# Kernel tuning notes

Hardware: AMD Instinct MI355X
Metric: run time of the kernel (lower is better)

## Reference

```python
import jax, jax.numpy as jnp
import numpy as np

N, F, LATENT = 4096, 64, 32
ENC = [128, 64]
DEC = [64, 96, 128]
B = 8


def _glorot(key, shape):
    s = jnp.sqrt(2.0 / (shape[0] + shape[-1]))
    return jax.random.normal(key, shape, jnp.float32) * s


def setup_inputs() -> dict:
    key = jax.random.key(0)
    ks = jax.random.split(key, 12)
    # Random symmetric graph (avg degree ~16), then spektral-style preprocessing:
    # normalized_laplacian: L = I - D^-1/2 A D^-1/2 ; rescale_laplacian(lmax=2): 2/lmax*L - I = L - I
    rng = np.random.default_rng(0)
    A = (rng.random((N, N)) < (16.0 / N)).astype(np.float32)
    A = np.maximum(A, A.T)
    np.fill_diagonal(A, 0.0)
    d = A.sum(1)
    dis = 1.0 / np.sqrt(np.maximum(d, 1.0))
    L = np.eye(N, dtype=np.float32) - dis[:, None] * A * dis[None, :]
    A0 = (L - np.eye(N, dtype=np.float32)).astype(np.float32)
    return dict(
        x=jax.random.normal(ks[0], (B, N, F), jnp.float32),
        eps=jax.random.normal(ks[1], (B, N // 4, LATENT), jnp.float32),
        A0=jnp.asarray(A0),
        W1=_glorot(ks[2], (F, ENC[0])), b1=jnp.zeros((ENC[0],), jnp.float32),
        p1=jax.random.normal(ks[3], (ENC[0],), jnp.float32),
        W2=_glorot(ks[4], (ENC[0], ENC[1])), b2=jnp.zeros((ENC[1],), jnp.float32),
        p2=jax.random.normal(ks[5], (ENC[1],), jnp.float32),
        Wlat=_glorot(ks[6], (ENC[1], 2 * LATENT)), blat=jnp.zeros((2 * LATENT,), jnp.float32),
        Wd0=_glorot(ks[7], (LATENT, DEC[0])), bd0=jnp.zeros((DEC[0],), jnp.float32),
        Wd1=_glorot(ks[8], (DEC[0], DEC[1])), bd1=jnp.zeros((DEC[1],), jnp.float32),
        Wd2=_glorot(ks[9], (DEC[1], DEC[2])), bd2=jnp.zeros((DEC[2],), jnp.float32),
        Wout=_glorot(ks[10], (DEC[2], F)), bout=jnp.zeros((F,), jnp.float32),
    )


def _gcn(x, A, W, b):
    # spektral GCNConv with pre-normalized adjacency: A @ x @ W + b
    return A @ (x @ W) + b


def _topk_pool(x, A, p):
    # spektral TopKPool (Graph U-Net): y = x.p/||p||, keep top ratio=0.5 nodes,
    # gate kept features with tanh(y), pool adjacency A' = A[idx][:, idx].
    y = x @ (p / jnp.linalg.norm(p))                 # [n]
    k = x.shape[0] // 2
    idx = jnp.sort(jax.lax.top_k(y, k)[1])           # node-order preserving
    xp = x[idx] * jnp.tanh(y[idx])[:, None]          # [k, c]
    Ap = A[idx][:, idx]                              # [k, k]
    return xp, Ap, idx


def _unpool(x, idx, n_old):
    # TopKUnpool: scatter pooled features back to their original node slots, zeros elsewhere.
    return jnp.zeros((n_old, x.shape[1]), x.dtype).at[idx].set(x)


def reference(x, eps, A0, W1, b1, p1, W2, b2, p2, Wlat, blat,
              Wd0, bd0, Wd1, bd1, Wd2, bd2, Wout, bout):
    def single(x1, eps1):
        # ---- encoder ----
        h = jax.nn.relu(_gcn(x1, A0, W1, b1))        # [N, 128]
        h, A1, idx1 = _topk_pool(h, A0, p1)          # [N/2, 128]
        h = jax.nn.relu(_gcn(h, A1, W2, b2))         # [N/2, 64]
        h, A2, idx2 = _topk_pool(h, A1, p2)          # [N/4, 64]
        hl = _gcn(h, A2, Wlat, blat)                 # [N/4, 2*LATENT]
        mean, logvar = jnp.split(hl, 2, axis=-1)
        # ---- reparameterize ----
        z = mean + jnp.exp(0.5 * logvar) * eps1
        # ---- decoder ----
        d = jax.nn.relu(_gcn(z, A2, Wd0, bd0))       # [N/4, 64]
        d = _unpool(d, idx2, N // 2)
        d = jax.nn.relu(_gcn(d, A1, Wd1, bd1))       # [N/2, 96]
        d = _unpool(d, idx1, N)
        d = jax.nn.relu(_gcn(d, A0, Wd2, bd2))       # [N, 128]
        out = jax.nn.softplus(_gcn(d, A0, Wout, bout))  # [N, F]
        return out, mean, logvar

    return jax.vmap(single)(x, eps)
```

## Files before the change

### kernel.cpp

```cpp
#include <hip/hip_runtime.h>
#include <hip/hip_bf16.h>

#define NN 4096
#define BB 8
#define LAT 32
#define ELLCAP 128

__global__ __launch_bounds__(256) void ell_build(const float* __restrict__ A,
                                                 int* __restrict__ col,
                                                 float* __restrict__ val,
                                                 int* __restrict__ nnz) {
  int w = threadIdx.x >> 6;
  int lane = threadIdx.x & 63;
  int row = blockIdx.x * 4 + w;
  const float* ar = A + (size_t)row * NN;
  int base = 0;
  for (int i = 0; i < NN; i += 256) {
    float4 a = *(const float4*)&ar[i + lane * 4];
    int cnt = (a.x != 0.f) + (a.y != 0.f) + (a.z != 0.f) + (a.w != 0.f);
    int x = cnt;
#pragma unroll
    for (int off = 1; off < 64; off <<= 1) {
      int y = __shfl_up(x, off, 64);
      if (lane >= off) x += y;
    }
    int total = __shfl(x, 63, 64);
    int p = base + x - cnt;
    float av[4] = {a.x, a.y, a.z, a.w};
#pragma unroll
    for (int u = 0; u < 4; u++) {
      if (av[u] != 0.f) {
        if (p < ELLCAP) {
          col[(size_t)row * ELLCAP + p] = i + lane * 4 + u;
          val[(size_t)row * ELLCAP + p] = av[u];
        }
        p++;
      }
    }
    base += total;
  }
  if (lane == 0) nnz[row] = base < ELLCAP ? base : ELLCAP;
}

__global__ void pnorm_kernel(const float* __restrict__ p1, const float* __restrict__ p2,
                             float* __restrict__ invn) {
  int lane = threadIdx.x;
  float s1 = 0.f, s2 = 0.f;
  for (int i = lane; i < 128; i += 64) s1 += p1[i] * p1[i];
  { float v = p2[lane]; s2 = v * v; }
  for (int off = 32; off; off >>= 1) { s1 += __shfl_down(s1, off); s2 += __shfl_down(s2, off); }
  if (lane == 0) { invn[0] = rsqrtf(s1); invn[1] = rsqrtf(s2); }
}

template <int CT>
__global__ __launch_bounds__(256) void gemm_kernel(
    const float* __restrict__ in, const float* __restrict__ W, float* __restrict__ out,
    int M, int K, long inB, long outB, const int* __restrict__ map, int mapB,
    const float* __restrict__ gateY, long gyB, const float* __restrict__ invn, int which) {
  const int C = CT * 32;
  const int KT = 32, LDI = KT + 4;
  extern __shared__ float lds[];
  float* Wl = lds;
  float* inT = lds + KT * C;
  int b = blockIdx.y;
  const float* inb = in + (size_t)b * inB;
  float* outb = out + (size_t)b * outB;
  const int* mapb = map ? map + (size_t)b * mapB : nullptr;
  int tx = threadIdx.x, ty = threadIdx.y;
  int row0 = blockIdx.x * 32;
  float acc[4][CT];
#pragma unroll
  for (int i = 0; i < 4; i++)
#pragma unroll
    for (int j = 0; j < CT; j++) acc[i][j] = 0.f;
  for (int kt = 0; kt < K; kt += KT) {
    int kc = (K - kt < KT) ? (K - kt) : KT;
    for (int r = ty; r < kc; r += 8)
      for (int c = tx; c < C; c += 32) Wl[r * C + c] = W[(size_t)(kt + r) * C + c];
    for (int r = ty; r < 32; r += 8) {
      int grow = row0 + r;
      int src = grow;
      if (mapb) src = mapb[grow];
      if (src >= 0) {
        float gate = 1.f;
        if (gateY) gate = tanhf(gateY[(size_t)b * gyB + src] * invn[which]);
        const float* ib = inb + (size_t)src * K + kt;
        for (int k = tx; k < kc; k += 32) inT[r * LDI + k] = ib[k] * gate;
      } else {
        for (int k = tx; k < kc; k += 32) inT[r * LDI + k] = 0.f;
      }
    }
    __syncthreads();
    for (int k = 0; k < kc; k += 4) {
      float4 a[4];
#pragma unroll
      for (int i = 0; i < 4; i++) a[i] = *(const float4*)&inT[(ty + i * 8) * LDI + k];
#pragma unroll
      for (int kk = 0; kk < 4; kk++) {
#pragma unroll
        for (int j = 0; j < CT; j++) {
          float w = Wl[(k + kk) * C + tx + j * 32];
#pragma unroll
          for (int i = 0; i < 4; i++) {
            float av = ((const float*)&a[i])[kk];
            acc[i][j] = fmaf(av, w, acc[i][j]);
          }
        }
      }
    }
    __syncthreads();
  }
#pragma unroll
  for (int i = 0; i < 4; i++) {
    int grow = row0 + ty + i * 8;
#pragma unroll
    for (int j = 0; j < CT; j++) outb[(size_t)grow * C + tx + j * 32] = acc[i][j];
  }
}

template <int C>
__global__ __launch_bounds__(128) void spmm_vec_kernel(
    const int* __restrict__ ecol, const float* __restrict__ evals, const int* __restrict__ ennz,
    const int* __restrict__ rowmap, int rowmapB,
    const int* __restrict__ colinv, int colinvB,
    const float* __restrict__ Y, long yB, const float* __restrict__ bias,
    float* __restrict__ out, long outB, int act,
    const float* __restrict__ eps, float* __restrict__ meanOut,
    float* __restrict__ logvarOut, float* __restrict__ zOut,
    const float* __restrict__ pvec, float* __restrict__ yOut, long yOutB) {
  constexpr int L = C / 4;
  constexpr int R = 128 / L;
  __shared__ int scol[R][ELLCAP];
  __shared__ float sval[R][ELLCAP];
  int bid = blockIdx.x;
  int rb = bid >> 3, b = bid & 7;
  int t = threadIdx.x;
  int rloc = t / L, lane = t % L;
  int row = rb * R + rloc;
  int grow = rowmap ? rowmap[(size_t)b * rowmapB + row] : row;
  int n = ennz[grow];
  const int* cp = ecol + (size_t)grow * ELLCAP;
  const float* vp = evals + (size_t)grow * ELLCAP;
  const int* ci = colinv ? colinv + (size_t)b * colinvB : nullptr;
  for (int e = lane; e < n; e += L) {
    int c = cp[e];
    int li = ci ? ci[c] : c;
    float w = vp[e];
    if (li < 0) { li = 0; w = 0.f; }
    scol[rloc][e] = li;
    sval[rloc][e] = w;
  }
  __syncthreads();
  const float* Yb = Y + (size_t)b * yB;
  float4 acc = {0.f, 0.f, 0.f, 0.f};
  int e = 0;
  for (; e + 8 <= n; e += 8) {
    float4 v[8];
    float w[8];
#pragma unroll
    for (int u = 0; u < 8; u++) {
      w[u] = sval[rloc][e + u];
      v[u] = *(const float4*)&Yb[(size_t)scol[rloc][e + u] * C + lane * 4];
    }
#pragma unroll
    for (int u = 0; u < 8; u++) {
      acc.x = fmaf(w[u], v[u].x, acc.x);
      acc.y = fmaf(w[u], v[u].y, acc.y);
      acc.z = fmaf(w[u], v[u].z, acc.z);
      acc.w = fmaf(w[u], v[u].w, acc.w);
    }
  }
  for (; e < n; e++) {
    float w = sval[rloc][e];
    float4 v = *(const float4*)&Yb[(size_t)scol[rloc][e] * C + lane * 4];
    acc.x = fmaf(w, v.x, acc.x);
    acc.y = fmaf(w, v.y, acc.y);
    acc.z = fmaf(w, v.z, acc.z);
    acc.w = fmaf(w, v.w, acc.w);
  }
  float4 bi = *(const float4*)&bias[lane * 4];
  acc.x += bi.x; acc.y += bi.y; acc.z += bi.z; acc.w += bi.w;
  if (act == 1) {
    acc.x = fmaxf(acc.x, 0.f); acc.y = fmaxf(acc.y, 0.f);
    acc.z = fmaxf(acc.z, 0.f); acc.w = fmaxf(acc.w, 0.f);
  } else if (act == 2) {
    acc.x = fmaxf(acc.x, 0.f) + log1pf(expf(-fabsf(acc.x)));
    acc.y = fmaxf(acc.y, 0.f) + log1pf(expf(-fabsf(acc.y)));
    acc.z = fmaxf(acc.z, 0.f) + log1pf(expf(-fabsf(acc.z)));
    acc.w = fmaxf(acc.w, 0.f) + log1pf(expf(-fabsf(acc.w)));
  } else if (act == 3) {
    int wl = t & 63;
    float4 lv;
    lv.x = __shfl(acc.x, wl + 8, 64);
    lv.y = __shfl(acc.y, wl + 8, 64);
    lv.z = __shfl(acc.z, wl + 8, 64);
    lv.w = __shfl(acc.w, wl + 8, 64);
    size_t o = ((size_t)b * 1024 + row) * LAT;
    if (lane < 8) {
      *(float4*)&meanOut[o + lane * 4] = acc;
      float4 ep = *(const float4*)&eps[o + lane * 4];
      float4 z;
      z.x = fmaf(expf(0.5f * lv.x), ep.x, acc.x);
      z.y = fmaf(expf(0.5f * lv.y), ep.y, acc.y);
      z.z = fmaf(expf(0.5f * lv.z), ep.z, acc.z);
      z.w = fmaf(expf(0.5f * lv.w), ep.w, acc.w);
      *(float4*)&zOut[o + lane * 4] = z;
    } else {
      *(float4*)&logvarOut[o + (lane - 8) * 4] = acc;
    }
    return;
  }
  *(float4*)&out[(size_t)b * outB + (size_t)row * C + lane * 4] = acc;
  if (yOut) {
    float4 pv = *(const float4*)&pvec[lane * 4];
    float part = acc.x * pv.x + acc.y * pv.y + acc.z * pv.z + acc.w * pv.w;
#pragma unroll
    for (int off = L / 2; off > 0; off >>= 1) part += __shfl_down(part, off, 64);
    if (lane == 0) yOut[(size_t)b * yOutB + row] = part;
  }
}

__global__ void spmm_kernel(
    const int* __restrict__ ecol, const float* __restrict__ evals, const int* __restrict__ ennz,
    const int* __restrict__ rowmap, int rowmapB,
    const int* __restrict__ colinv, int colinvB,
    const float* __restrict__ Y, long yB, const float* __restrict__ bias,
    float* __restrict__ out, long outB, int C, int act) {
  __shared__ int scol[ELLCAP];
  __shared__ float sval[ELLCAP];
  int bid = blockIdx.x;
  int row = bid >> 3, b = bid & 7;
  int t = threadIdx.x;
  int grow = rowmap ? rowmap[(size_t)b * rowmapB + row] : row;
  int n = ennz[grow];
  const int* cp = ecol + (size_t)grow * ELLCAP;
  const float* vp = evals + (size_t)grow * ELLCAP;
  const int* ci = colinv ? colinv + (size_t)b * colinvB : nullptr;
  for (int e = t; e < n; e += C) {
    int c = cp[e];
    int li = ci ? ci[c] : c;
    float w = vp[e];
    if (li < 0) { li = 0; w = 0.f; }
    scol[e] = li;
    sval[e] = w;
  }
  __syncthreads();
  const float* Yb = Y + (size_t)b * yB;
  float acc = 0.f;
  int e = 0;
  for (; e + 8 <= n; e += 8) {
    const float* ap[8];
    float w[8], pv[8];
#pragma unroll
    for (int u = 0; u < 8; u++) {
      ap[u] = Yb + (size_t)scol[e + u] * C + t;
      w[u] = sval[e + u];
    }
#pragma unroll
    for (int u = 0; u < 8; u++) pv[u] = *ap[u];
#pragma unroll
    for (int u = 0; u < 8; u++) acc = fmaf(w[u], pv[u], acc);
  }
  for (; e < n; e++) acc = fmaf(sval[e], Yb[(size_t)scol[e] * C + t], acc);
  acc += bias[t];
  if (act == 1) acc = fmaxf(acc, 0.f);
  out[(size_t)b * outB + (size_t)row * C + t] = acc;
}

__global__ __launch_bounds__(1024) void topk_kernel(
    const float* __restrict__ yIn, int yB, int n, int k,
    const int* __restrict__ prevIdx, int prevB,
    int* __restrict__ idxLoc, int idxB,
    int* __restrict__ invLoc, int invB,
    int* __restrict__ gIdx, int gIdxB,
    int* __restrict__ gInv, int gInvB) {
  __shared__ unsigned int sk[4096];
  __shared__ unsigned int hist[256];
  __shared__ int si[1024];
  __shared__ int s_bin, s_cum;
  int b = blockIdx.x, tid = threadIdx.x;
  const float* y = yIn + (size_t)b * yB;
  for (int i = tid; i < n; i += 1024) {
    unsigned u = __float_as_uint(y[i]);
    sk[i] = (u & 0x80000000u) ? ~u : (u | 0x80000000u);
  }
  int* invb = invLoc + (size_t)b * invB;
  for (int i = tid; i < n; i += 1024) invb[i] = -1;
  int* ginvb = gInv ? gInv + (size_t)b * gInvB : nullptr;
  if (ginvb)
    for (int i = tid; i < NN; i += 1024) ginvb[i] = -1;
  __syncthreads();
  unsigned prefix = 0;
  int kneed = k, countGt = 0;
  for (int shift = 24; shift >= 0; shift -= 8) {
    if (tid < 256) hist[tid] = 0;
    __syncthreads();
    unsigned pmask = (shift == 24) ? 0u : (0xFFFFFFFFu << (shift + 8));
    for (int i = tid; i < n; i += 1024) {
      unsigned key = sk[i];
      if ((key & pmask) == prefix) atomicAdd(&hist[(key >> shift) & 255], 1u);
    }
    __syncthreads();
    if (tid < 256) si[tid] = (int)hist[tid];
    __syncthreads();
    for (int off = 1; off < 256; off <<= 1) {
      int v = 0;
      if (tid < 256) { v = si[tid]; if (tid + off < 256) v += si[tid + off]; }
      __syncthreads();
      if (tid < 256) si[tid] = v;
      __syncthreads();
    }
    if (tid < 256) {
      int cumAbove = (tid < 255) ? si[tid + 1] : 0;
      if (cumAbove < kneed && kneed <= cumAbove + (int)hist[tid]) {
        s_bin = tid;
        s_cum = cumAbove;
      }
    }
    __syncthreads();
    int bin = s_bin, cumAbove = s_cum;
    countGt += cumAbove;
    kneed -= cumAbove;
    prefix |= ((unsigned)bin << shift);
    __syncthreads();
  }
  unsigned tkey = prefix;
  int needEq = k - countGt;
  int ipt = n >> 10;
  int i0 = tid * ipt;
  int locGt = 0, locEq = 0;
  for (int u = 0; u < ipt; u++) {
    unsigned key = sk[i0 + u];
    locGt += (key > tkey) ? 1 : 0;
    locEq += (key == tkey) ? 1 : 0;
  }
  int comb = (locGt << 13) | locEq;
  si[tid] = comb;
  __syncthreads();
  for (int off = 1; off < 1024; off <<= 1) {
    int vv = si[tid];
    int add = (tid >= off) ? si[tid - off] : 0;
    __syncthreads();
    si[tid] = vv + add;
    __syncthreads();
  }
  int excl = si[tid] - comb;
  int gtB = excl >> 13;
  int eqB = excl & 0x1FFF;
  int* idxb = idxLoc + (size_t)b * idxB;
  int* gidxb = gIdx ? gIdx + (size_t)b * gIdxB : nullptr;
  const int* prevb = prevIdx ? prevIdx + (size_t)b * prevB : nullptr;
  for (int u = 0; u < ipt; u++) {
    int i = i0 + u;
    unsigned key = sk[i];
    bool g = key > tkey;
    bool e = (key == tkey);
    bool sel = g || (e && eqB < needEq);
    if (sel) {
      int pos = gtB + (eqB < needEq ? eqB : needEq);
      idxb[pos] = i;
      invb[i] = pos;
      int gi = prevb ? prevb[i] : i;
      if (gidxb) gidxb[pos] = gi;
      if (ginvb) ginvb[gi] = pos;
    }
    gtB += g ? 1 : 0;
    eqB += e ? 1 : 0;
  }
}

static inline void launch_gemm(const float* in, const float* W, float* out, int M, int K, int C,
                               long inB, long outB, const int* map, int mapB, hipStream_t s,
                               const float* gateY = nullptr, long gyB = 0,
                               const float* invn = nullptr, int which = 0) {
  dim3 g(M / 32, BB), bl(32, 8);
  size_t lds = (size_t)(32 * C + 32 * 36) * 4;
  if (C == 64)
    gemm_kernel<2><<<g, bl, lds, s>>>(in, W, out, M, K, inB, outB, map, mapB, gateY, gyB, invn, which);
  else if (C == 96)
    gemm_kernel<3><<<g, bl, lds, s>>>(in, W, out, M, K, inB, outB, map, mapB, gateY, gyB, invn, which);
  else
    gemm_kernel<4><<<g, bl, lds, s>>>(in, W, out, M, K, inB, outB, map, mapB, gateY, gyB, invn, which);
}

static inline void launch_spmm(const int* ecol, const float* evals, const int* ennz,
                               const int* rowmap, int rowmapB, const int* colinv, int colinvB,
                               const float* Y, long yB, const float* bias, float* out, long outB,
                               int M, int C, int act, hipStream_t s,
                               const float* eps = nullptr, float* meanOut = nullptr,
                               float* lvOut = nullptr, float* zOut = nullptr,
                               const float* pvec = nullptr, float* yOut = nullptr, long yOutB = 0) {
  if (C == 128) {
    spmm_vec_kernel<128><<<dim3((M / 4) * BB), dim3(128), 0, s>>>(
        ecol, evals, ennz, rowmap, rowmapB, colinv, colinvB, Y, yB, bias, out, outB, act,
        eps, meanOut, lvOut, zOut, pvec, yOut, yOutB);
  } else if (C == 64) {
    spmm_vec_kernel<64><<<dim3((M / 8) * BB), dim3(128), 0, s>>>(
        ecol, evals, ennz, rowmap, rowmapB, colinv, colinvB, Y, yB, bias, out, outB, act,
        eps, meanOut, lvOut, zOut, pvec, yOut, yOutB);
  } else {
    spmm_kernel<<<dim3(M * BB), dim3(C), 0, s>>>(ecol, evals, ennz, rowmap, rowmapB, colinv,
                                                 colinvB, Y, yB, bias, out, outB, C, act);
  }
}

extern "C" void kernel_launch(void* const* d_in, const int* in_sizes, int n_in,
                              void* d_out, int out_size, void* d_ws, size_t ws_size,
                              hipStream_t stream) {
  const float* x = (const float*)d_in[0];
  const float* eps = (const float*)d_in[1];
  const float* A0 = (const float*)d_in[2];
  const float* W1 = (const float*)d_in[3];
  const float* b1 = (const float*)d_in[4];
  const float* p1 = (const float*)d_in[5];
  const float* W2 = (const float*)d_in[6];
  const float* b2 = (const float*)d_in[7];
  const float* p2 = (const float*)d_in[8];
  const float* Wlat = (const float*)d_in[9];
  const float* blat = (const float*)d_in[10];
  const float* Wd0 = (const float*)d_in[11];
  const float* bd0 = (const float*)d_in[12];
  const float* Wd1 = (const float*)d_in[13];
  const float* bd1 = (const float*)d_in[14];
  const float* Wd2 = (const float*)d_in[15];
  const float* bd2 = (const float*)d_in[16];
  const float* Wout = (const float*)d_in[17];
  const float* bout = (const float*)d_in[18];
  float* outp = (float*)d_out;
  float* meanOut = outp + (size_t)BB * 4096 * 64;
  float* logvarOut = meanOut + (size_t)BB * 1024 * 32;

  char* ws = (char*)d_ws;
  size_t off = 0;
  auto alloc = [&](size_t bytes) {
    void* p = ws + off;
    off = (off + bytes + 255) & ~(size_t)255;
    return p;
  };
  int* ell_col = (int*)alloc((size_t)NN * ELLCAP * 4);
  float* ell_val = (float*)alloc((size_t)NN * ELLCAP * 4);
  int* ell_nnz = (int*)alloc((size_t)NN * 4);
  float* invn = (float*)alloc(256);
  float* t0 = (float*)alloc((size_t)BB * 4096 * 128 * 4);
  float* t1 = (float*)alloc((size_t)BB * 4096 * 128 * 4);
  float* t2 = (float*)alloc((size_t)BB * 4096 * 128 * 4);
  float* y1 = (float*)alloc((size_t)BB * 4096 * 4);
  float* y2 = (float*)alloc((size_t)BB * 2048 * 4);
  int* idx1 = (int*)alloc((size_t)BB * 2048 * 4);
  int* inv1 = (int*)alloc((size_t)BB * 4096 * 4);
  int* idx2 = (int*)alloc((size_t)BB * 1024 * 4);
  int* inv2 = (int*)alloc((size_t)BB * 2048 * 4);
  int* gidx2 = (int*)alloc((size_t)BB * 1024 * 4);
  int* ginv2 = (int*)alloc((size_t)BB * 4096 * 4);
  float* zbuf = (float*)alloc((size_t)BB * 1024 * 32 * 4);

  ell_build<<<dim3(NN / 4), dim3(256), 0, stream>>>(A0, ell_col, ell_val, ell_nnz);
  pnorm_kernel<<<dim3(1), dim3(64), 0, stream>>>(p1, p2, invn);

  launch_gemm(x, W1, t0, 4096, 64, 128, 4096l * 64, 4096l * 128, nullptr, 0, stream);
  launch_spmm(ell_col, ell_val, ell_nnz, nullptr, 0, nullptr, 0, t0, 4096l * 128, b1, t1,
              4096l * 128, 4096, 128, 1, stream, nullptr, nullptr, nullptr, nullptr,
              p1, y1, 4096);
  topk_kernel<<<dim3(BB), dim3(1024), 0, stream>>>(y1, 4096, 4096, 2048, nullptr, 0, idx1, 2048,
                                                   inv1, 4096, nullptr, 0, nullptr, 0);

  launch_gemm(t1, W2, t0, 2048, 128, 64, 4096l * 128, 2048l * 64, idx1, 2048, stream,
              y1, 4096, invn, 0);
  launch_spmm(ell_col, ell_val, ell_nnz, idx1, 2048, inv1, 4096, t0, 2048l * 64, b2, t1,
              2048l * 64, 2048, 64, 1, stream, nullptr, nullptr, nullptr, nullptr,
              p2, y2, 2048);
  topk_kernel<<<dim3(BB), dim3(1024), 0, stream>>>(y2, 2048, 2048, 1024, idx1, 2048, idx2, 1024,
                                                   inv2, 2048, gidx2, 1024, ginv2, 4096);

  launch_gemm(t1, Wlat, t0, 1024, 64, 64, 2048l * 64, 1024l * 64, idx2, 1024, stream,
              y2, 2048, invn, 1);
  launch_spmm(ell_col, ell_val, ell_nnz, gidx2, 1024, ginv2, 4096, t0, 1024l * 64, blat, nullptr,
              0, 1024, 64, 3, stream, eps, meanOut, logvarOut, zbuf);

  launch_gemm(zbuf, Wd0, t0, 1024, 32, 64, 1024l * 32, 1024l * 64, nullptr, 0, stream);
  launch_spmm(ell_col, ell_val, ell_nnz, gidx2, 1024, ginv2, 4096, t0, 1024l * 64, bd0, t2,
              1024l * 64, 1024, 64, 1, stream);
  launch_gemm(t2, Wd1, t0, 2048, 64, 96, 1024l * 64, 2048l * 96, inv2, 2048, stream);
  launch_spmm(ell_col, ell_val, ell_nnz, idx1, 2048, inv1, 4096, t0, 2048l * 96, bd1, t1,
              2048l * 96, 2048, 96, 1, stream);
  launch_gemm(t1, Wd2, t0, 4096, 96, 128, 2048l * 96, 4096l * 128, inv1, 4096, stream);
  launch_spmm(ell_col, ell_val, ell_nnz, nullptr, 0, nullptr, 0, t0, 4096l * 128, bd2, t2,
              4096l * 128, 4096, 128, 1, stream);
  launch_gemm(t2, Wout, t0, 4096, 128, 64, 4096l * 128, 4096l * 64, nullptr, 0, stream);
  launch_spmm(ell_col, ell_val, ell_nnz, nullptr, 0, nullptr, 0, t0, 4096l * 64, bout, outp,
              4096l * 64, 4096, 64, 2, stream);
}
```

Baseline: 452.1 us.

## Vectorize GEMM weight/output access and add multi-row float4 SpMM for width 96

The dense GEMM now gives each thread contiguous column groups, so weight tile loads, LDS reads and output stores use float2/float4. Its grid is flattened so the batch index is interleaved with the row block. The scalar one-row-per-block SpMM used for the 96-wide layer is replaced by a kernel that handles 8 rows per block with 24 lanes each loading float4, which cuts launch count and widens memory transactions. The GEMM also drops the partial-K handling and assumes K is a multiple of 32, which holds for the shapes used here.

After: 395.3 us. 1.14x faster.

```diff
diff --git a/kernel.cpp b/kernel.cpp
--- a/kernel.cpp
+++ b/kernel.cpp
@@ -52,31 +52,41 @@
   if (lane == 0) { invn[0] = rsqrtf(s1); invn[1] = rsqrtf(s2); }
 }
 
-template <int CT>
+template <int VW>
 __global__ __launch_bounds__(256) void gemm_kernel(
     const float* __restrict__ in, const float* __restrict__ W, float* __restrict__ out,
     int M, int K, long inB, long outB, const int* __restrict__ map, int mapB,
     const float* __restrict__ gateY, long gyB, const float* __restrict__ invn, int which) {
-  const int C = CT * 32;
+  const int C = VW * 32;
   const int KT = 32, LDI = KT + 4;
   extern __shared__ float lds[];
   float* Wl = lds;
   float* inT = lds + KT * C;
-  int b = blockIdx.y;
+  int bid = blockIdx.x;
+  int b = bid & 7;
+  int row0 = (bid >> 3) * 32;
   const float* inb = in + (size_t)b * inB;
   float* outb = out + (size_t)b * outB;
   const int* mapb = map ? map + (size_t)b * mapB : nullptr;
   int tx = threadIdx.x, ty = threadIdx.y;
-  int row0 = blockIdx.x * 32;
-  float acc[4][CT];
+  float acc[4][VW];
 #pragma unroll
   for (int i = 0; i < 4; i++)
 #pragma unroll
-    for (int j = 0; j < CT; j++) acc[i][j] = 0.f;
+    for (int j = 0; j < VW; j++) acc[i][j] = 0.f;
   for (int kt = 0; kt < K; kt += KT) {
-    int kc = (K - kt < KT) ? (K - kt) : KT;
-    for (int r = ty; r < kc; r += 8)
-      for (int c = tx; c < C; c += 32) Wl[r * C + c] = W[(size_t)(kt + r) * C + c];
+    for (int r = ty; r < KT; r += 8) {
+      const float* ws = &W[(size_t)(kt + r) * C + tx * VW];
+      float* wd = &Wl[r * C + tx * VW];
+      if constexpr (VW == 4) {
+        *(float4*)wd = *(const float4*)ws;
+      } else if constexpr (VW == 2) {
+        *(float2*)wd = *(const float2*)ws;
+      } else {
+#pragma unroll
+        for (int j = 0; j < VW; j++) wd[j] = ws[j];
+      }
+    }
     for (int r = ty; r < 32; r += 8) {
       int grow = row0 + r;
       int src = grow;
@@ -85,26 +95,34 @@
         float gate = 1.f;
         if (gateY) gate = tanhf(gateY[(size_t)b * gyB + src] * invn[which]);
         const float* ib = inb + (size_t)src * K + kt;
-        for (int k = tx; k < kc; k += 32) inT[r * LDI + k] = ib[k] * gate;
+        inT[r * LDI + tx] = ib[tx] * gate;
       } else {
-        for (int k = tx; k < kc; k += 32) inT[r * LDI + k] = 0.f;
+        inT[r * LDI + tx] = 0.f;
       }
     }
     __syncthreads();
-    for (int k = 0; k < kc; k += 4) {
+    for (int k = 0; k < KT; k += 4) {
       float4 a[4];
 #pragma unroll
       for (int i = 0; i < 4; i++) a[i] = *(const float4*)&inT[(ty + i * 8) * LDI + k];
 #pragma unroll
       for (int kk = 0; kk < 4; kk++) {
-#pragma unroll
-        for (int j = 0; j < CT; j++) {
-          float w = Wl[(k + kk) * C + tx + j * 32];
-#pragma unroll
-          for (int i = 0; i < 4; i++) {
-            float av = ((const float*)&a[i])[kk];
-            acc[i][j] = fmaf(av, w, acc[i][j]);
-          }
+        float w[VW];
+        if constexpr (VW == 4) {
+          float4 wv = *(const float4*)&Wl[(k + kk) * C + tx * 4];
+          w[0] = wv.x; w[1] = wv.y; w[2] = wv.z; w[3] = wv.w;
+        } else if constexpr (VW == 2) {
+          float2 wv = *(const float2*)&Wl[(k + kk) * C + tx * 2];
+          w[0] = wv.x; w[1] = wv.y;
+        } else {
+#pragma unroll
+          for (int j = 0; j < VW; j++) w[j] = Wl[(k + kk) * C + tx * VW + j];
+        }
+#pragma unroll
+        for (int i = 0; i < 4; i++) {
+          float av = ((const float*)&a[i])[kk];
+#pragma unroll
+          for (int j = 0; j < VW; j++) acc[i][j] = fmaf(av, w[j], acc[i][j]);
         }
       }
     }
@@ -113,8 +131,17 @@
 #pragma unroll
   for (int i = 0; i < 4; i++) {
     int grow = row0 + ty + i * 8;
-#pragma unroll
-    for (int j = 0; j < CT; j++) outb[(size_t)grow * C + tx + j * 32] = acc[i][j];
+    float* od = &outb[(size_t)grow * C + tx * VW];
+    if constexpr (VW == 4) {
+      float4 o = {acc[i][0], acc[i][1], acc[i][2], acc[i][3]};
+      *(float4*)od = o;
+    } else if constexpr (VW == 2) {
+      float2 o = {acc[i][0], acc[i][1]};
+      *(float2*)od = o;
+    } else {
+#pragma unroll
+      for (int j = 0; j < VW; j++) od[j] = acc[i][j];
+    }
   }
 }
 
@@ -220,51 +247,68 @@
   }
 }
 
-__global__ void spmm_kernel(
+__global__ __launch_bounds__(192) void spmm_vec96_kernel(
     const int* __restrict__ ecol, const float* __restrict__ evals, const int* __restrict__ ennz,
     const int* __restrict__ rowmap, int rowmapB,
     const int* __restrict__ colinv, int colinvB,
     const float* __restrict__ Y, long yB, const float* __restrict__ bias,
-    float* __restrict__ out, long outB, int C, int act) {
-  __shared__ int scol[ELLCAP];
-  __shared__ float sval[ELLCAP];
+    float* __restrict__ out, long outB, int act) {
+  constexpr int L = 24, R = 8, C = 96;
+  __shared__ int scol[R][ELLCAP];
+  __shared__ float sval[R][ELLCAP];
   int bid = blockIdx.x;
-  int row = bid >> 3, b = bid & 7;
+  int rb = bid >> 3, b = bid & 7;
   int t = threadIdx.x;
+  int rloc = t / L, lane = t % L;
+  int row = rb * R + rloc;
   int grow = rowmap ? rowmap[(size_t)b * rowmapB + row] : row;
   int n = ennz[grow];
   const int* cp = ecol + (size_t)grow * ELLCAP;
   const float* vp = evals + (size_t)grow * ELLCAP;
   const int* ci = colinv ? colinv + (size_t)b * colinvB : nullptr;
-  for (int e = t; e < n; e += C) {
+  for (int e = lane; e < n; e += L) {
     int c = cp[e];
     int li = ci ? ci[c] : c;
     float w = vp[e];
     if (li < 0) { li = 0; w = 0.f; }
-    scol[e] = li;
-    sval[e] = w;
+    scol[rloc][e] = li;
+    sval[rloc][e] = w;
   }
   __syncthreads();
   const float* Yb = Y + (size_t)b * yB;
-  float acc = 0.f;
+  float4 acc = {0.f, 0.f, 0.f, 0.f};
   int e = 0;
   for (; e + 8 <= n; e += 8) {
-    const float* ap[8];
-    float w[8], pv[8];
+    float4 v[8];
+    float w[8];
 #pragma unroll
     for (int u = 0; u < 8; u++) {
-      ap[u] = Yb + (size_t)scol[e + u] * C + t;
-      w[u] = sval[e + u];
-    }
-#pragma unroll
-    for (int u = 0; u < 8; u++) pv[u] = *ap[u];
-#pragma unroll
-    for (int u = 0; u < 8; u++) acc = fmaf(w[u], pv[u], acc);
-  }
-  for (; e < n; e++) acc = fmaf(sval[e], Yb[(size_t)scol[e] * C + t], acc);
-  acc += bias[t];
-  if (act == 1) acc = fmaxf(acc, 0.f);
-  out[(size_t)b * outB + (size_t)row * C + t] = acc;
+      w[u] = sval[rloc][e + u];
+      v[u] = *(const float4*)&Yb[(size_t)scol[rloc][e + u] * C + lane * 4];
+    }
+#pragma unroll
+    for (int u = 0; u < 8; u++) {
+      acc.x = fmaf(w[u], v[u].x, acc.x);
+      acc.y = fmaf(w[u], v[u].y, acc.y);
+      acc.z = fmaf(w[u], v[u].z, acc.z);
+      acc.w = fmaf(w[u], v[u].w, acc.w);
+    }
+  }
+  for (; e < n; e++) {
+    float w = sval[rloc][e];
+    float4 v = *(const float4*)&Yb[(size_t)scol[rloc][e] * C + lane * 4];
+    acc.x = fmaf(w, v.x, acc.x);
+    acc.y = fmaf(w, v.y, acc.y);
+    acc.z = fmaf(w, v.z, acc.z);
+    acc.w = fmaf(w, v.w, acc.w);
+  }
+  float4 bi = *(const float4*)&bias[lane * 4];
+  acc.x += bi.x; acc.y += bi.y; acc.z += bi.z; acc.w += bi.w;
+  if (act == 1) {
+    acc.x = fmaxf(acc.x, 0.f); acc.y = fmaxf(acc.y, 0.f);
+    acc.z = fmaxf(acc.z, 0.f); acc.w = fmaxf(acc.w, 0.f);
+  }
+  *(float4*)&out[(size_t)b * outB + (size_t)row * C + lane * 4] = acc;
 }
 
 __global__ __launch_bounds__(1024) void topk_kernel(
@@ -373,7 +417,7 @@
                                long inB, long outB, const int* map, int mapB, hipStream_t s,
                                const float* gateY = nullptr, long gyB = 0,
                                const float* invn = nullptr, int which = 0) {
-  dim3 g(M / 32, BB), bl(32, 8);
+  dim3 g((M / 32) * BB), bl(32, 8);
   size_t lds = (size_t)(32 * C + 32 * 36) * 4;
   if (C == 64)
     gemm_kernel<2><<<g, bl, lds, s>>>(in, W, out, M, K, inB, outB, map, mapB, gateY, gyB, invn, which);
@@ -399,8 +443,8 @@
         ecol, evals, ennz, rowmap, rowmapB, colinv, colinvB, Y, yB, bias, out, outB, act,
         eps, meanOut, lvOut, zOut, pvec, yOut, yOutB);
   } else {
-    spmm_kernel<<<dim3(M * BB), dim3(C), 0, s>>>(ecol, evals, ennz, rowmap, rowmapB, colinv,
-                                                 colinvB, Y, yB, bias, out, outB, C, act);
+    spmm_vec96_kernel<<<dim3((M / 8) * BB), dim3(192), 0, s>>>(
+        ecol, evals, ennz, rowmap, rowmapB, colinv, colinvB, Y, yB, bias, out, outB, act);
   }
 }
 
```
